# Optimization experiments

Measured on AMD Instinct MI355X. Metric: run time of the kernel, lower is better.

Reference implementation:

```python
import jax, jax.numpy as jnp
import numpy as np

MAX_LR = 0.01  # max_learning_rate
NS_A, NS_B, NS_C = 3.4445, -4.7750, 2.0315  # muon Newton-Schulz quintic coefficients


def newtonschulz5(G, steps=5, eps=1e-7):
    # Orthogonalize the last two dims of G (batched over leading dims).
    transpose = G.shape[-2] > G.shape[-1]
    X = jnp.swapaxes(G, -2, -1) if transpose else G
    X = X / (jnp.linalg.norm(X, axis=(-2, -1), keepdims=True) + eps)
    for _ in range(steps):
        A = X @ jnp.swapaxes(X, -2, -1)
        Bm = NS_B * A + NS_C * (A @ A)
        X = NS_A * X + Bm @ X
    return jnp.swapaxes(X, -2, -1) if transpose else X


def setup_inputs() -> dict:
    key = jax.random.key(0)
    ks = jax.random.split(key, 9)
    B, N, D, H, DH = 4, 1024, 1024, 8, 64
    s = D ** -0.5  # scale fast-weight init for numerical sanity (math unchanged)
    return {
        'tokens': jax.random.normal(ks[0], (B, N, D), jnp.float32),
        'wq': jax.random.normal(ks[1], (H, D, DH), jnp.float32) * s,
        'wk': jax.random.normal(ks[2], (H, D, DH), jnp.float32) * s,
        'wv': jax.random.normal(ks[3], (H, D, DH), jnp.float32) * s,
        'wo': jax.random.normal(ks[4], (H, DH, D), jnp.float32) * s,
        'w_lr': jax.random.normal(ks[5], (D, 2), jnp.float32) * 0.02,      # to_learning_rate (no bias)
        'w_target': jax.random.normal(ks[6], (D, D), jnp.float32) * 0.02,  # to_target_values linear (no bias)
        'w_gates': jax.random.normal(ks[7], (D, H), jnp.float32) * 0.02,   # to_gates linear (no bias)
        'rms_w': jnp.ones((D,), jnp.float32),                              # RMSNorm weight
    }


def reference(tokens, wq, wk, wv, wo, w_lr, w_target, w_gates, rms_w):
    N = tokens.shape[1]
    scale = wq.shape[-1] ** -0.5
    eps = jnp.finfo(tokens.dtype).eps

    # RMSNorm
    t = tokens * jax.lax.rsqrt(jnp.mean(tokens * tokens, -1, keepdims=True) + eps) * rms_w

    # gates: b n h -> b h n 1
    gates = jnp.swapaxes(jax.nn.sigmoid(t @ w_gates), -2, -1)[..., None]

    # per-batch fast weights == shared params (past_mem=None), broadcast over b via einsum
    q = jnp.einsum('bnd,hde->bhne', t, wq)
    k = jnp.einsum('bnd,hde->bhne', t, wk)
    v = jnp.einsum('bnd,hde->bhne', t, wv)

    score = jnp.einsum('bhie,bhje->bhij', q, k) * scale
    causal_mask = jnp.triu(jnp.ones((N, N), bool), 1)
    score = jnp.where(causal_mask, -jnp.finfo(score.dtype).max, score)
    attn = jax.nn.softmax(score, axis=-1)
    out = jnp.einsum('bhij,bhje->bhie', attn, v) * gates
    pred_values = jnp.einsum('bhne,hed->bnd', out, wo)

    # target values: linear + LayerNorm (no affine) on shifted tokens
    tv = t[:, 1:] @ w_target
    tv = (tv - tv.mean(-1, keepdims=True)) * jax.lax.rsqrt(tv.var(-1, keepdims=True) + 1e-5)

    # drop last position everywhere
    ts = t[:, :-1]
    pv = pred_values[:, :-1]
    o = out[:, :, :-1]
    g = gates[:, :, :-1]
    a = attn[:, :, :-1, :-1]
    qs, ks_, vs = q[:, :, :-1], k[:, :, :-1], v[:, :, :-1]

    lrs = jax.nn.sigmoid(ts @ w_lr) * MAX_LR  # b (n-1) 2
    lr, mlr = lrs[..., 0], lrs[..., 1]

    # hand-derived backward through the attention fast-weight readout
    error = tv - pv
    dout = jnp.einsum('bnd,hed->bhne', error, wo)
    du = dout * g
    delta = jnp.sum(dout * o, -1, keepdims=True)
    dv = jnp.einsum('bhij,bhie->bhje', a, du)
    dattn = jnp.einsum('bhje,bhie->bhij', vs, du)
    dscore = scale * a * (dattn - delta)
    dq = jnp.einsum('bhje,bhij->bhie', ks_, dscore)
    dk = jnp.einsum('bhie,bhij->bhje', qs, dscore)

    t_qk = ts * lr[..., None]
    t_v = ts * mlr[..., None]
    o_wo = o * mlr[:, None, :, None]

    dwq = jnp.einsum('bhie,bid->bhde', dq, t_qk)
    dwk = jnp.einsum('bhje,bjd->bhde', dk, t_qk)
    dwv = jnp.einsum('bhje,bjd->bhde', dv, t_v)
    dwo = jnp.einsum('bnd,bhne->bhed', error, o_wo)

    dwv = newtonschulz5(dwv)  # muon orthogonalization
    dwo = newtonschulz5(dwo)

    return pred_values, dwq, dwk, dwv, dwo
```

## Files before the change

### kernel.cpp

```cpp
#include <hip/hip_runtime.h>
#include <hip/hip_bf16.h>
#include <math.h>

#define BB 4
#define NN 1024
#define DD 1024
#define HH 8
#define DH 64
#define NSR 1023

#define NS_Ac 3.4445f
#define NS_Bc (-4.775f)
#define NS_Cc 2.0315f

typedef short bf16x8 __attribute__((ext_vector_type(8)));
typedef float f32x4 __attribute__((ext_vector_type(4)));
#define MFMA16(a,b,c) __builtin_amdgcn_mfma_f32_16x16x32_bf16(a,b,c,0,0,0)

#define QS 72
#define TS 40
#define GS 40

static __device__ __forceinline__ float ldin(const void* p, size_t i, int f) {
  return f ? ((const float*)p)[i] : __bfloat162float(((const __hip_bfloat16*)p)[i]);
}
static __device__ __forceinline__ void stout(void* p, size_t i, float v, int f) {
  if (f) ((float*)p)[i] = v;
  else   ((__hip_bfloat16*)p)[i] = __float2bfloat16(v);
}
static __device__ __forceinline__ short f2bs(float x) {
  union { float f; unsigned u; } a; a.f = x;
  unsigned r = a.u + 0x7fffu + ((a.u >> 16) & 1u);
  return (short)(r >> 16);
}
static __device__ __forceinline__ float bs2f(short s) {
  union { unsigned u; float f; } a; a.u = ((unsigned)(unsigned short)s) << 16;
  return a.f;
}
static __device__ __forceinline__ f32x4 fz4() { f32x4 z = {0.f,0.f,0.f,0.f}; return z; }
static __device__ __forceinline__ bf16x8 bz8() { bf16x8 z = {0,0,0,0,0,0,0,0}; return z; }

static __device__ __forceinline__ void mm64(const short* __restrict__ Ah, const short* __restrict__ Al,
                                            const short* __restrict__ Bh, const short* __restrict__ Bl,
                                            f32x4* acc, int w, int l15, int quad) {
#pragma unroll
  for (int kc = 0; kc < 64; kc += 32) {
    bf16x8 ah = *(const bf16x8*)&Ah[(w*16 + l15)*QS + kc + quad*8];
    bf16x8 al = *(const bf16x8*)&Al[(w*16 + l15)*QS + kc + quad*8];
#pragma unroll
    for (int es = 0; es < 4; es++) {
      bf16x8 bh = *(const bf16x8*)&Bh[(es*16 + l15)*QS + kc + quad*8];
      bf16x8 bl = *(const bf16x8*)&Bl[(es*16 + l15)*QS + kc + quad*8];
      acc[es] = MFMA16(ah, bh, acc[es]);
      acc[es] = MFMA16(ah, bl, acc[es]);
      acc[es] = MFMA16(al, bh, acc[es]);
    }
  }
}
static __device__ __forceinline__ void st_hl(short* __restrict__ Dh, short* __restrict__ Dl,
                                             const f32x4* v, int w, int l15, int quad) {
#pragma unroll
  for (int es = 0; es < 4; es++)
#pragma unroll
    for (int rr = 0; rr < 4; rr++) {
      int row = w*16 + quad*4 + rr, col = es*16 + l15;
      float x = v[es][rr];
      short h = f2bs(x);
      Dh[row*QS + col] = h;
      Dl[row*QS + col] = f2bs(x - bs2f(h));
    }
}

__global__ __launch_bounds__(256) void k_prep(
    const void* wq, const void* wk, const void* wv,
    const void* w_target, const void* wo, const void* w_lr, const void* w_gates, const void* rms_w,
    short* __restrict__ BqkvT, short* __restrict__ wtT, short* __restrict__ woT2,
    short* __restrict__ wo_bf, float* __restrict__ lrw, float* __restrict__ gw,
    float* __restrict__ rms_f, int* __restrict__ flag)
{
  const int f = (((const unsigned short*)rms_w)[0] == 0x3F80) ? 0 : 1;
  int bx = blockIdx.x; int tid = threadIdx.x;
  if (bx >= 768) {
    if (bx < 812) {
      if (bx == 768 && tid == 0) *flag = f;
      int idx = (bx - 768)*256 + tid;
      if (idx < 2048) lrw[idx] = ldin(w_lr, idx, f);
      else if (idx < 10240) gw[idx-2048] = ldin(w_gates, idx-2048, f);
      else if (idx < 11264) rms_f[idx-10240] = ldin(rms_w, idx-10240, f);
    } else {
      size_t base = (size_t)(bx - 812)*1024;
#pragma unroll
      for (int j = 0; j < 4; j++) {
        size_t i2 = base + tid + 256*j;
        wo_bf[i2] = f2bs(ldin(wo, i2, f));
      }
    }
    return;
  }
  const void* src; short* dst; int sld, dld, srow0, scol0, drow0; size_t soff = 0;
  if (bx < 384) {
    int x = bx & 15, y = bx >> 4;
    int n0 = y*64; int which = n0 >> 9, h = (n0 >> 6) & 7;
    src = (which==0) ? wq : (which==1) ? wk : wv;
    soff = (size_t)h*65536;
    sld = 64; dld = 1024; srow0 = x*64; scol0 = 0; drow0 = n0; dst = BqkvT;
  } else if (bx < 640) {
    int r = bx - 384; int x = r & 15, y = r >> 4;
    src = w_target; dst = wtT; sld = 1024; dld = 1024;
    srow0 = x*64; scol0 = y*64; drow0 = scol0;
  } else {
    int r = bx - 640; int x = r & 7, y = r >> 3;
    src = wo; dst = woT2; sld = 1024; dld = 512;
    srow0 = x*64; scol0 = y*64; drow0 = scol0;
  }
  __shared__ float T[64][65];
  int r4 = tid >> 4, c4 = (tid & 15)*4;
  for (int rr = r4; rr < 64; rr += 16)
#pragma unroll
    for (int j = 0; j < 4; j++)
      T[rr][c4+j] = ldin(src, soff + (size_t)(srow0+rr)*sld + scol0 + c4 + j, f);
  __syncthreads();
  int dc = tid >> 2, seg = tid & 3;
  bf16x8 o1, o2;
#pragma unroll
  for (int j = 0; j < 8; j++) { o1[j] = f2bs(T[seg*16+j][dc]); o2[j] = f2bs(T[seg*16+8+j][dc]); }
  *(bf16x8*)&dst[(size_t)(drow0+dc)*dld + srow0 + seg*16]     = o1;
  *(bf16x8*)&dst[(size_t)(drow0+dc)*dld + srow0 + seg*16 + 8] = o2;
}

__global__ __launch_bounds__(256) void k_transp(
    const float* __restrict__ src, size_t sStepZ, int sld,
    short* __restrict__ dst, size_t dStepZ, int dld,
    const float* __restrict__ coef, int zIsBh, int nz)
{
  int z = blockIdx.z;
  const float* sb = src + (size_t)z*sStepZ;
  short* db = dst + (size_t)z*dStepZ;
  const float* cb = coef ? coef + (size_t)(zIsBh ? (z>>3) : z)*1024 : (const float*)0;
  int x0 = blockIdx.x*64, y0 = blockIdx.y*64;
  __shared__ float T[64][65];
  int tid = threadIdx.x;
  int r4 = tid >> 4, c4 = (tid & 15)*4;
  for (int rr = r4; rr < 64; rr += 16) {
    int rg = x0 + rr;
    bool val = rg < nz;
    float cf = val ? (cb ? cb[rg] : 1.f) : 0.f;
    float4 v = val ? *(const float4*)&sb[(size_t)rg*sld + y0 + c4] : make_float4(0,0,0,0);
    T[rr][c4+0] = v.x*cf; T[rr][c4+1] = v.y*cf; T[rr][c4+2] = v.z*cf; T[rr][c4+3] = v.w*cf;
  }
  __syncthreads();
  int dc = tid >> 2, seg = tid & 3;
  bf16x8 o1, o2;
#pragma unroll
  for (int j = 0; j < 8; j++) { o1[j] = f2bs(T[seg*16+j][dc]); o2[j] = f2bs(T[seg*16+8+j][dc]); }
  *(bf16x8*)&db[(size_t)(y0+dc)*dld + x0 + seg*16]     = o1;
  *(bf16x8*)&db[(size_t)(y0+dc)*dld + x0 + seg*16 + 8] = o2;
}

__global__ __launch_bounds__(256) void k_transp5(
    const float* __restrict__ dq, const float* __restrict__ dk, const float* __restrict__ dv,
    const float* __restrict__ predf, const float* __restrict__ o,
    short* __restrict__ dqT, short* __restrict__ dkT, short* __restrict__ dvT,
    short* __restrict__ errT, short* __restrict__ oT,
    const float* __restrict__ lr, const float* __restrict__ mlr)
{
  int bx = blockIdx.x;
  const float* src; short* dst; const float* cb; int sld, dld, x0, y0;
  size_t sStep, dStep; int z;
  if (bx < 1536) {
    int which = bx >> 9; int r = bx & 511;
    z = r >> 4; x0 = (r & 15)*64; y0 = 0;
    sld = 64; dld = 1024; sStep = 65536; dStep = 65536;
    if (which == 0)      { src = dq; dst = dqT; cb = lr; }
    else if (which == 1) { src = dk; dst = dkT; cb = lr; }
    else                 { src = dv; dst = dvT; cb = mlr; }
    cb += (size_t)(z >> 3)*1024;
  } else if (bx < 2560) {
    int r = bx - 1536; z = r >> 8; x0 = (r & 15)*64; y0 = ((r >> 4) & 15)*64;
    src = predf; dst = errT; cb = (const float*)0;
    sld = 1024; dld = 1024; sStep = 1048576; dStep = 1048576;
  } else {
    int r = bx - 2560; z = r >> 7; x0 = (r & 15)*64; y0 = ((r >> 4) & 7)*64;
    src = o; dst = oT; cb = mlr + (size_t)z*1024;
    sld = 512; dld = 1024; sStep = 524288; dStep = 524288;
  }
  src += (size_t)z*sStep; dst += (size_t)z*dStep;
  __shared__ float T[64][65];
  int tid = threadIdx.x;
  int r4 = tid >> 4, c4 = (tid & 15)*4;
  for (int rr = r4; rr < 64; rr += 16) {
    int rg = x0 + rr;
    bool val = rg < 1023;
    float cf = val ? (cb ? cb[rg] : 1.f) : 0.f;
    float4 v = val ? *(const float4*)&src[(size_t)rg*sld + y0 + c4] : make_float4(0,0,0,0);
    T[rr][c4+0] = v.x*cf; T[rr][c4+1] = v.y*cf; T[rr][c4+2] = v.z*cf; T[rr][c4+3] = v.w*cf;
  }
  __syncthreads();
  int dc = tid >> 2, seg = tid & 3;
  bf16x8 o1, o2;
#pragma unroll
  for (int j = 0; j < 8; j++) { o1[j] = f2bs(T[seg*16+j][dc]); o2[j] = f2bs(T[seg*16+8+j][dc]); }
  *(bf16x8*)&dst[(size_t)(y0+dc)*dld + x0 + seg*16]     = o1;
  *(bf16x8*)&dst[(size_t)(y0+dc)*dld + x0 + seg*16 + 8] = o2;
}

__global__ void k_rmsnorm(const void* __restrict__ tokens, const float* __restrict__ rms_f,
                          const float* __restrict__ gw, const float* __restrict__ lrw,
                          float* __restrict__ t, short* __restrict__ t_bf,
                          float* __restrict__ gates, float* __restrict__ lr, float* __restrict__ mlr,
                          const int* __restrict__ flag) {
  const int f = *flag;
  int row = blockIdx.x;
  int b = row >> 10, n = row & 1023;
  __shared__ float red[256];
  __shared__ float red2[4][10];
  float xv[4]; float acc = 0.f;
#pragma unroll
  for (int i = 0; i < 4; i++) {
    xv[i] = ldin(tokens, (size_t)row*DD + threadIdx.x + 256*i, f);
    acc += xv[i]*xv[i];
  }
  red[threadIdx.x] = acc; __syncthreads();
  for (int s = 128; s > 0; s >>= 1) { if (threadIdx.x < s) red[threadIdx.x] += red[threadIdx.x+s]; __syncthreads(); }
  float r = rsqrtf(red[0] / DD + 1.1920929e-07f);
  float a10[10] = {0,0,0,0,0,0,0,0,0,0};
#pragma unroll
  for (int i = 0; i < 4; i++) {
    int d = threadIdx.x + 256*i;
    float v = xv[i] * r * rms_f[d];
    t[(size_t)row*DD + d] = v;
    t_bf[(size_t)row*DD + d] = f2bs(v);
#pragma unroll
    for (int h = 0; h < HH; h++) a10[h] += v * gw[d*HH + h];
    a10[8] += v * lrw[d*2];
    a10[9] += v * lrw[d*2+1];
  }
  int lane = threadIdx.x & 63, w = threadIdx.x >> 6;
#pragma unroll
  for (int c = 0; c < 10; c++) {
    float a = a10[c];
    for (int s = 32; s > 0; s >>= 1) a += __shfl_xor(a, s, 64);
    if (lane == 0) red2[w][c] = a;
  }
  __syncthreads();
  if (threadIdx.x < 10) {
    int c = threadIdx.x;
    float sum = red2[0][c]+red2[1][c]+red2[2][c]+red2[3][c];
    float sg = 1.f / (1.f + __expf(-sum));
    if (c < 8)      gates[((size_t)b*HH + c)*NN + n] = sg;
    else if (c == 8) lr[row]  = sg * 0.01f;
    else             mlr[row] = sg * 0.01f;
  }
}

__global__ __launch_bounds__(256) void k_gemm2(
    const short* __restrict__ A, const short* __restrict__ B,
    int lda, int ldb, int K, int M, int rowmode, int ep,
    float* __restrict__ O0, short* __restrict__ OS, void* __restrict__ OD,
    short* __restrict__ VT, const float* __restrict__ gates, const int* __restrict__ flag)
{
  int m0 = blockIdx.x*128, n0 = blockIdx.y*128;
  __shared__ __align__(16) short sm2[17408];
  short* As = sm2;
  short* Bs = sm2 + 5120;
  int tid = threadIdx.x;
  int lane = tid & 63, w = tid >> 6;
  int wr = w >> 1, wc = w & 1;
  int l15 = lane & 15, quad = lane >> 4;
  int row = tid >> 1, col16 = (tid & 1)*16;
  int r = m0 + row;
  int arow;
  if (rowmode == 1)      { int b = r / 1023; arow = r + b + 1; }
  else if (rowmode == 2) { int b = r / 1023; arow = r + b; }
  else arow = r;
  bool aval = (r < M);
  const short* Ap = A + (size_t)arow*lda + col16;
  const short* Bp = B + (size_t)(n0+row)*ldb + col16;
  f32x4 acc[4][4];
#pragma unroll
  for (int mi = 0; mi < 4; mi++)
#pragma unroll
    for (int ni = 0; ni < 4; ni++) acc[mi][ni] = fz4();
  bf16x8 av0 = aval ? *(const bf16x8*)(Ap) : bz8();
  bf16x8 av1 = aval ? *(const bf16x8*)(Ap + 8) : bz8();
  bf16x8 bv0 = *(const bf16x8*)(Bp);
  bf16x8 bv1 = *(const bf16x8*)(Bp + 8);
  for (int kb = 0; kb < K; kb += 32) {
    __syncthreads();
    *(bf16x8*)&As[row*GS + col16]     = av0;
    *(bf16x8*)&As[row*GS + col16 + 8] = av1;
    *(bf16x8*)&Bs[row*GS + col16]     = bv0;
    *(bf16x8*)&Bs[row*GS + col16 + 8] = bv1;
    __syncthreads();
    if (kb + 32 < K) {
      av0 = aval ? *(const bf16x8*)(Ap + kb + 32) : bz8();
      av1 = aval ? *(const bf16x8*)(Ap + kb + 40) : bz8();
      bv0 = *(const bf16x8*)(Bp + kb + 32);
      bv1 = *(const bf16x8*)(Bp + kb + 40);
    }
    bf16x8 afr[4], bfr[4];
#pragma unroll
    for (int mi = 0; mi < 4; mi++)
      afr[mi] = *(const bf16x8*)&As[(wr*64 + mi*16 + l15)*GS + quad*8];
#pragma unroll
    for (int ni = 0; ni < 4; ni++)
      bfr[ni] = *(const bf16x8*)&Bs[(wc*64 + ni*16 + l15)*GS + quad*8];
#pragma unroll
    for (int mi = 0; mi < 4; mi++)
#pragma unroll
      for (int ni = 0; ni < 4; ni++)
        acc[mi][ni] = MFMA16(afr[mi], bfr[ni], acc[mi][ni]);
  }
  const int f = flag ? *flag : 1;
#pragma unroll
  for (int mi = 0; mi < 4; mi++)
#pragma unroll
    for (int ni = 0; ni < 4; ni++)
#pragma unroll
      for (int rix = 0; rix < 4; rix++) {
        int rr = m0 + wr*64 + mi*16 + quad*4 + rix;
        if (rr >= M) continue;
        int c = n0 + wc*64 + ni*16 + l15;
        float val = acc[mi][ni][rix];
        if (ep == 0) {
          int which = c >> 9; int h = (c >> 6) & 7; int e = c & 63;
          int b = rr >> 10; int n = rr & 1023;
          OS[(size_t)which*2097152 + (((size_t)b*8 + h)*1024 + n)*64 + e] = f2bs(val);
        } else if (ep == 1) {
          O0[(size_t)rr*1024 + c] = val;
          stout(OD, (size_t)rr*1024 + c, val, f);
        } else if (ep == 2) {
          O0[(size_t)rr*1024 + c] = val;
        } else {
          int b = rr / 1023; int n = rr % 1023;
          int h = c >> 6;
          float g = gates[((size_t)b*8 + h)*1024 + n];
          OS[((size_t)b*1024 + n)*512 + c] = f2bs(val * g);
        }
      }
  if (ep == 0 && n0 >= 1024) {
    short* ST = sm2;
    __syncthreads();
#pragma unroll
    for (int mi = 0; mi < 4; mi++)
#pragma unroll
      for (int ni = 0; ni < 4; ni++)
#pragma unroll
        for (int rix = 0; rix < 4; rix++) {
          int ml = wr*64 + mi*16 + quad*4 + rix;
          int cl = wc*64 + ni*16 + l15;
          int mo = ml + ((ml >> 6) << 3);
          ST[cl*136 + mo] = f2bs(acc[mi][ni][rix]);
        }
    __syncthreads();
    int r2 = tid >> 1;
    int sg = tid & 1;
    int cg = n0 + r2;
    int h = (cg >> 6) & 7;
    int e = cg & 63;
    int b = m0 >> 10;
    int bh = b*8 + h;
    size_t dst = ((size_t)bh*64 + e)*1024 + (m0 & 1023) + sg*64;
    int so = r2*136 + sg*72;
#pragma unroll
    for (int j = 0; j < 64; j += 8)
      *(bf16x8*)&VT[dst + j] = *(const bf16x8*)&ST[so + j];
  }
}

__global__ __launch_bounds__(256) void k_gemm_bf(
    const short* __restrict__ A, const short* __restrict__ B,
    int lda, int ldb, int K, int M, int rowmode, int ep,
    size_t aStepBh, size_t aStepB, size_t bStepBh, size_t bStepB,
    float* __restrict__ O0, short* __restrict__ OS, void* __restrict__ OD,
    size_t out_off, const float* __restrict__ gates, const int* __restrict__ flag,
    const short* __restrict__ A2, const short* __restrict__ B2,
    size_t bStepB2, size_t out_off2, int ldb2)
{
  int z = blockIdx.z;
  const short* Au = A; const short* Bu = B;
  size_t bStepBv = bStepB; size_t out_offv = out_off;
  int epv = ep; int ldbv = ldb;
  if (ep == 4 && z >= 32) { Bu = B2; out_offv = out_off2; z -= 32; }
  if (ep == 5 && z >= 32) { Au = A2; Bu = B2; bStepBv = bStepB2; ldbv = ldb2; epv = 6; z -= 32; }
  int zb = z >> 3;
  const short* Ab = Au + (size_t)z*aStepBh + (size_t)zb*aStepB;
  const short* Bb = Bu + (size_t)z*bStepBh + (size_t)zb*bStepBv;
  int m0 = blockIdx.x*64, n0 = blockIdx.y*64;
  __shared__ __align__(16) short AsBs[5120];
  short* As = AsBs;
  short* Bs = AsBs + 2560;
  int tid = threadIdx.x;
  int lane = tid & 63, w = tid >> 6;
  int l15 = lane & 15, quad = lane >> 4;
  int row = tid >> 2, col8 = (tid & 3)*8;
  int r = m0 + row;
  int arow;
  if (rowmode == 1)      { int b = r / 1023; arow = r + b + 1; }
  else if (rowmode == 2) { int b = r / 1023; arow = r + b; }
  else arow = r;
  bool aval = (r < M);
  const short* Ap = Ab + (size_t)arow*lda + col8;
  const short* Bp = Bb + (size_t)(n0+row)*ldbv + col8;
  f32x4 acc[4] = {fz4(),fz4(),fz4(),fz4()};
  bf16x8 av = aval ? *(const bf16x8*)(Ap) : bz8();
  bf16x8 bv = *(const bf16x8*)(Bp);
  for (int kb = 0; kb < K; kb += 32) {
    __syncthreads();
    *(bf16x8*)&As[row*GS + col8] = av;
    *(bf16x8*)&Bs[row*GS + col8] = bv;
    __syncthreads();
    if (kb + 32 < K) {
      av = aval ? *(const bf16x8*)(Ap + kb + 32) : bz8();
      bv = *(const bf16x8*)(Bp + kb + 32);
    }
    bf16x8 afr = *(const bf16x8*)&As[(w*16 + l15)*GS + quad*8];
#pragma unroll
    for (int es = 0; es < 4; es++) {
      bf16x8 bfr = *(const bf16x8*)&Bs[(es*16 + l15)*GS + quad*8];
      acc[es] = MFMA16(afr, bfr, acc[es]);
    }
  }
  const int f = flag ? *flag : 1;
#pragma unroll
  for (int es = 0; es < 4; es++) {
#pragma unroll
    for (int rix = 0; rix < 4; rix++) {
      int rr = m0 + w*16 + quad*4 + rix;
      if (rr >= M) continue;
      int c = n0 + es*16 + l15;
      float val = acc[es][rix];
      if (epv == 4) {
        stout(OD, out_offv + ((size_t)z*1024 + rr)*64 + c, val, f);
      } else if (epv == 5) {
        O0[((size_t)z*64 + rr)*1024 + c] = val;
      } else if (epv == 6) {
        O0[((size_t)(32 + z)*64 + rr)*1024 + c] = val;
      }
    }
  }
}

__global__ __launch_bounds__(256) void k_attn_fwd(
    const short* __restrict__ qb, const short* __restrict__ kb, const short* __restrict__ vbT,
    const float* __restrict__ gates,
    float* __restrict__ o, short* __restrict__ o_bf,
    float* __restrict__ mrow, float* __restrict__ lrow)
{
  int pp = blockIdx.x >> 8;
  int xx = (blockIdx.x >> 5) & 7;
  int bh = blockIdx.x & 31;
  int it = pp ? xx : (15 - xx);
  int i0 = it*64;
  int b = bh >> 3, h = bh & 7;
  __shared__ __align__(16) short Qs[64*QS];
  __shared__ __align__(16) short Ks[32*QS];
  __shared__ __align__(16) short VsT[64*TS];
  __shared__ __align__(16) short Ps[64*TS];
  int tid = threadIdx.x;
  int lane = tid & 63, w = tid >> 6;
  int l15 = lane & 15, quad = lane >> 4;
  int sr = tid >> 3, sc = (tid & 7) * 8;
  int sr2 = tid >> 2, sc2 = (tid & 3) * 8;
  int rsw = (l15 >> 2) & 3;
  for (int rr = sr; rr < 64; rr += 32)
    *(bf16x8*)&Qs[rr*QS + sc] = *(const bf16x8*)&qb[((size_t)bh*1024 + i0 + rr)*64 + sc];
  f32x4 oa[4] = {fz4(),fz4(),fz4(),fz4()};
  float m_st[4] = {-1e30f,-1e30f,-1e30f,-1e30f};
  float l_st[4] = {0.f,0.f,0.f,0.f};
  int jiters = 2*it + 2;
  bf16x8 rk = *(const bf16x8*)&kb[((size_t)bh*1024 + sr)*64 + sc];
  bf16x8 rv = *(const bf16x8*)&vbT[((size_t)bh*64 + sr2)*1024 + sc2];
  for (int jc = 0; jc < jiters; jc++) {
    int j0 = jc*32;
    __syncthreads();
    *(bf16x8*)&Ks[sr*QS + sc]    = rk;
    *(bf16x8*)&VsT[sr2*TS + sc2] = rv;
    __syncthreads();
    if (jc + 1 < jiters) {
      int j1 = j0 + 32;
      rk = *(const bf16x8*)&kb[((size_t)bh*1024 + j1 + sr)*64 + sc];
      rv = *(const bf16x8*)&vbT[((size_t)bh*64 + sr2)*1024 + j1 + sc2];
    }
    f32x4 sa[2] = {fz4(),fz4()};
#pragma unroll
    for (int kc = 0; kc < 64; kc += 32) {
      bf16x8 afr = *(const bf16x8*)&Qs[(w*16 + l15)*QS + kc + quad*8];
#pragma unroll
      for (int ni = 0; ni < 2; ni++) {
        bf16x8 bfr = *(const bf16x8*)&Ks[(ni*16 + l15)*QS + kc + quad*8];
        sa[ni] = MFMA16(afr, bfr, sa[ni]);
      }
    }
#pragma unroll
    for (int r = 0; r < 4; r++) {
      int gi = i0 + w*16 + quad*4 + r;
      float s0 = sa[0][r]*0.125f, s1 = sa[1][r]*0.125f;
      if (j0 + l15 > gi)      s0 = -1e30f;
      if (j0 + 16 + l15 > gi) s1 = -1e30f;
      float rm = fmaxf(s0, s1);
      rm = fmaxf(rm, __shfl_xor(rm, 1, 64));
      rm = fmaxf(rm, __shfl_xor(rm, 2, 64));
      rm = fmaxf(rm, __shfl_xor(rm, 4, 64));
      rm = fmaxf(rm, __shfl_xor(rm, 8, 64));
      float m_new = fmaxf(m_st[r], rm);
      float alpha = __expf(m_st[r] - m_new);
      float p0 = __expf(s0 - m_new), p1 = __expf(s1 - m_new);
      float rs = p0 + p1;
      rs += __shfl_xor(rs, 1, 64);
      rs += __shfl_xor(rs, 2, 64);
      rs += __shfl_xor(rs, 4, 64);
      rs += __shfl_xor(rs, 8, 64);
      l_st[r] = l_st[r]*alpha + rs;
      m_st[r] = m_new;
#pragma unroll
      for (int es = 0; es < 4; es++) oa[es][r] *= alpha;
      int rowp = w*16 + quad*4 + r;
      int lo3 = l15 & 7, g0 = l15 >> 3;
      Ps[rowp*TS + ((( g0      ^ quad) << 3) | lo3)] = f2bs(p0);
      Ps[rowp*TS + ((((g0 | 2) ^ quad) << 3) | lo3)] = f2bs(p1);
    }
    bf16x8 pa = *(const bf16x8*)&Ps[(w*16 + l15)*TS + ((quad ^ rsw) << 3)];
#pragma unroll
    for (int es = 0; es < 4; es++) {
      bf16x8 bv = *(const bf16x8*)&VsT[(es*16 + l15)*TS + quad*8];
      oa[es] = MFMA16(pa, bv, oa[es]);
    }
  }
#pragma unroll
  for (int r = 0; r < 4; r++) {
    int gi = i0 + w*16 + quad*4 + r;
    float g = gates[(size_t)bh*1024 + gi] / l_st[r];
#pragma unroll
    for (int es = 0; es < 4; es++) {
      float val = oa[es][r] * g;
      size_t oi = ((size_t)b*1024 + gi)*512 + h*64 + es*16 + l15;
      o[oi] = val;
      o_bf[oi] = f2bs(val);
    }
    if (l15 == 0) {
      mrow[(size_t)bh*1024 + gi] = m_st[r];
      lrow[(size_t)bh*1024 + gi] = l_st[r];
    }
  }
}

__global__ void k_lnsub(const float* __restrict__ tvbuf, float* __restrict__ predf,
                        short* __restrict__ err_bf) {
  int r = blockIdx.x; int b = r / 1023; int prow = r + b;
  const float* tvr = tvbuf + (size_t)r*1024;
  __shared__ float red[256];
  float s1 = 0.f, s2 = 0.f;
  float xv[4];
#pragma unroll
  for (int i = 0; i < 4; i++) {
    xv[i] = tvr[threadIdx.x + 256*i];
    s1 += xv[i]; s2 += xv[i]*xv[i];
  }
  red[threadIdx.x] = s1; __syncthreads();
  for (int s = 128; s > 0; s >>= 1){ if (threadIdx.x < s) red[threadIdx.x] += red[threadIdx.x+s]; __syncthreads(); }
  float mean = red[0] / 1024.f; __syncthreads();
  red[threadIdx.x] = s2; __syncthreads();
  for (int s = 128; s > 0; s >>= 1){ if (threadIdx.x < s) red[threadIdx.x] += red[threadIdx.x+s]; __syncthreads(); }
  float var = red[0]/1024.f - mean*mean;
  float rstd = rsqrtf(var + 1e-5f);
  float* er = predf + (size_t)prow*1024;
#pragma unroll
  for (int i = 0; i < 4; i++) {
    int d = threadIdx.x + 256*i;
    float e = (xv[i]-mean)*rstd - er[d];
    er[d] = e;
    err_bf[(size_t)prow*1024 + d] = f2bs(e);
  }
// ... 405 lines not shown
    __syncthreads();
  }
#pragma unroll
  for (int es = 0; es < 4; es++)
#pragma unroll
    for (int rr = 0; rr < 4; rr++) {
      int row = w*16 + quad*4 + rr, col = es*16 + l15;
      M5[(size_t)m*4096 + row*64 + col] = bs2f(Mhi[row*QS + col]) + bs2f(Mlo[row*QS + col]);
    }
  if (tid == 0) rbuf[m] = r_;
}

__global__ __launch_bounds__(256) void k_ns_apply(const float* __restrict__ Xsrc, const float* __restrict__ M5,
                                                  const float* __restrict__ rbuf, void* __restrict__ d_outv,
                                                  size_t off_dwv, size_t off_dwo, const int* __restrict__ flag) {
  int m = blockIdx.x, cs = blockIdx.y;
  const float* Xm = Xsrc + (size_t)m*DH*DD;
  const int f = *flag;
  float r_ = rbuf[m];
  __shared__ __align__(16) short Mhi[4608], Mlo[4608], XThi[4608], XTlo[4608];
  __shared__ float Sf[64*65];
  int tid = threadIdx.x;
  int lane = tid & 63, w = tid >> 6;
  int l15 = lane & 15, quad = lane >> 4;
  int srow = tid >> 2, scol = (tid & 3)*8;
  for (int i = tid; i < 4096; i += 256) {
    float v = M5[(size_t)m*4096 + i];
    int rowi = i >> 6, coli = i & 63;
    short h = f2bs(v);
    Mhi[rowi*QS + coli] = h;
    Mlo[rowi*QS + coli] = f2bs(v - bs2f(h));
  }
  int cbase = cs*256;
  float4 d1 = *(const float4*)&Xm[(size_t)srow*1024 + cbase + scol];
  float4 d2 = *(const float4*)&Xm[(size_t)srow*1024 + cbase + scol + 4];
  float4 d3 = *(const float4*)&Xm[(size_t)srow*1024 + cbase + scol + 32];
  float4 d4 = *(const float4*)&Xm[(size_t)srow*1024 + cbase + scol + 36];
  for (int cc = 0; cc < 256; cc += 64) {
    int c0 = cbase + cc;
    __syncthreads();
    {
      float xv0[8] = {d1.x,d1.y,d1.z,d1.w,d2.x,d2.y,d2.z,d2.w};
      float xv1[8] = {d3.x,d3.y,d3.z,d3.w,d4.x,d4.y,d4.z,d4.w};
#pragma unroll
      for (int j = 0; j < 8; j++) {
        int n0 = scol + j;
        short h0 = f2bs(xv0[j]);
        XThi[n0*QS + srow] = h0;
        XTlo[n0*QS + srow] = f2bs(xv0[j] - bs2f(h0));
        int n1 = scol + 32 + j;
        short h1 = f2bs(xv1[j]);
        XThi[n1*QS + srow] = h1;
        XTlo[n1*QS + srow] = f2bs(xv1[j] - bs2f(h1));
      }
    }
    __syncthreads();
    if (cc + 64 < 256) {
      d1 = *(const float4*)&Xm[(size_t)srow*1024 + c0 + 64 + scol];
      d2 = *(const float4*)&Xm[(size_t)srow*1024 + c0 + 64 + scol + 4];
      d3 = *(const float4*)&Xm[(size_t)srow*1024 + c0 + 64 + scol + 32];
      d4 = *(const float4*)&Xm[(size_t)srow*1024 + c0 + 64 + scol + 36];
    }
    f32x4 u4[4] = {fz4(),fz4(),fz4(),fz4()};
    mm64(Mhi, Mlo, XThi, XTlo, u4, w, l15, quad);
    if (m >= 32) {
#pragma unroll
      for (int es = 0; es < 4; es++)
#pragma unroll
        for (int rr = 0; rr < 4; rr++) {
          int row = w*16 + quad*4 + rr, col = c0 + es*16 + l15;
          stout(d_outv, off_dwo + (size_t)(m-32)*65536 + (size_t)row*1024 + col, r_*u4[es][rr], f);
        }
    } else {
#pragma unroll
      for (int es = 0; es < 4; es++)
#pragma unroll
        for (int rr = 0; rr < 4; rr++) {
          int row = w*16 + quad*4 + rr, col = es*16 + l15;
          Sf[col*65 + row] = r_*u4[es][rr];
        }
      __syncthreads();
      int dl = tid >> 2, e0 = (tid & 3)*16;
      size_t ob = off_dwv + (size_t)m*65536 + (size_t)(c0 + dl)*64 + e0;
#pragma unroll
      for (int j = 0; j < 16; j++)
        stout(d_outv, ob + j, Sf[dl*65 + e0 + j], f);
    }
  }
}

extern "C" void kernel_launch(void* const* d_in, const int* in_sizes, int n_in,
                              void* d_out, int out_size, void* d_ws, size_t ws_size,
                              hipStream_t stream) {
  const void* tokens   = d_in[0];
  const void* wq       = d_in[1];
  const void* wk       = d_in[2];
  const void* wv       = d_in[3];
  const void* wo       = d_in[4];
  const void* w_lr     = d_in[5];
  const void* w_target = d_in[6];
  const void* w_gates  = d_in[7];
  const void* rms_w    = d_in[8];

  const size_t off_dwq  = 4194304;
  const size_t off_dwk  = 6291456;
  const size_t off_dwv  = 8388608;
  const size_t off_dwo  = 10485760;

  float* ws = (float*)d_ws;
  float* t_    = ws;
  float* tvbuf = ws;
  short* errT  = (short*)ws;
  short* oT    = (short*)(ws + 2097152);
  short* t_bf  = (short*)(ws + 4194304);
  short* err_bf= (short*)(ws + 4194304);
  short* tT    = (short*)(ws + 6291456);
  short* qb    = (short*)(ws + 8388608);
  short* kbuf  = qb + 2097152;
  short* vbuf  = qb + 4194304;
  short* dqT   = (short*)(ws + 8388608);
  short* dkT   = dqT + 2097152;
  short* dvT   = dqT + 4194304;
  float* o_    = ws + 11534336;
  short* o_bf  = (short*)(ws + 13631488);
  short* du_bf = (short*)(ws + 13631488);
  float* predf = ws + 14680064;
  float* Xns   = ws + 14680064;
  short* BqkvT = (short*)(ws + 18874368);
  short* wtT   = (short*)(ws + 19660800);
  short* woT2  = (short*)(ws + 20185088);
  short* wo_bf = (short*)(ws + 20447232);
  float* gw    = ws + 20709376;
  float* lrw   = ws + 20717568;
  float* rms_f = ws + 20719616;
  float* dv_   = ws + 18874368;
  float* dk_   = ws + 20971520;
  float* dq_   = ws + 23068672;
  float* gates_= ws + 25165824;
  float* mrow_ = ws + 25198592;
  float* lrow_ = ws + 25231360;
  float* delta_= ws + 25264128;
  float* lr_   = ws + 25296896;
  float* mlr_  = ws + 25300992;
  int*   flag_ = (int*)(ws + 25305088);
  short* vbT = (short*)(ws + 3145728);
  short* duT = (short*)(ws + 3145728);
  short* kbT = (short*)(ws + 4194304);
  short* qbT = (short*)ws;
  float* Gpart  = ws + 18874368;
  float* M5b    = ws + 19922944;
  float* rbuf   = ws + 20185088;
  float* sspart = ws + 20185152;

  hipLaunchKernelGGL(k_prep, dim3(1324), dim3(256), 0, stream, wq, wk, wv, w_target, wo, w_lr, w_gates, rms_w,
                     BqkvT, wtT, woT2, wo_bf, lrw, gw, rms_f, flag_);
  hipLaunchKernelGGL(k_rmsnorm, dim3(BB*NN), dim3(256), 0, stream, tokens, rms_f, gw, lrw,
                     t_, t_bf, gates_, lr_, mlr_, flag_);
  hipLaunchKernelGGL(k_transp, dim3(64,16,1), dim3(256), 0, stream, t_, (size_t)0, 1024, tT, (size_t)0, 4096, (const float*)nullptr, 0, 4096);

  hipLaunchKernelGGL(k_gemm2, dim3(32,12), dim3(256), 0, stream, t_bf, BqkvT, 1024, 1024, 1024, 4096, 0, 0,
                     (float*)nullptr, qb, (void*)nullptr, vbT, (const float*)nullptr, flag_);
  hipLaunchKernelGGL(k_attn_fwd, dim3(512), dim3(256), 0, stream, qb, kbuf, vbT, gates_, o_, o_bf, mrow_, lrow_);
  hipLaunchKernelGGL(k_gemm2, dim3(32,8), dim3(256), 0, stream, o_bf, woT2, 512, 512, 512, 4096, 0, 1,
                     predf, (short*)nullptr, d_out, (short*)nullptr, (const float*)nullptr, flag_);
  hipLaunchKernelGGL(k_gemm2, dim3(32,8), dim3(256), 0, stream, t_bf, wtT, 1024, 1024, 1024, 4092, 1, 2,
                     tvbuf, (short*)nullptr, (void*)nullptr, (short*)nullptr, (const float*)nullptr, flag_);
  hipLaunchKernelGGL(k_lnsub, dim3(BB*NSR), dim3(256), 0, stream, tvbuf, predf, err_bf);
  hipLaunchKernelGGL(k_gemm2, dim3(32,4), dim3(256), 0, stream, err_bf, wo_bf, 1024, 1024, 1024, 4092, 2, 3,
                     (float*)nullptr, du_bf, (void*)nullptr, (short*)nullptr, gates_, flag_);
  hipLaunchKernelGGL(k_t16, dim3(1536 + BB*NSR), dim3(256), 0, stream, (const short*)qb, (const short*)du_bf,
                     kbT, duT, qbT, o_, gates_, delta_);
  hipLaunchKernelGGL(k_bwd, dim3(1024), dim3(256), 0, stream, qb, kbuf, vbuf, du_bf, qbT, duT, kbT,
                     mrow_, lrow_, delta_, dv_, dk_, dq_);
  hipLaunchKernelGGL(k_transp5, dim3(3072), dim3(256), 0, stream, dq_, dk_, dv_, predf, o_,
                     dqT, dkT, dvT, errT, oT, lr_, mlr_);
  hipLaunchKernelGGL(k_gemm_bf, dim3(16,1,64), dim3(256), 0, stream, tT, dqT, 4096, 1024, 1024, 1024, 0, 4,
                     (size_t)0,(size_t)1024,(size_t)65536,(size_t)0, (float*)nullptr, (short*)nullptr, d_out, off_dwq,
                     (const float*)nullptr, flag_, (const short*)nullptr, (const short*)dkT, (size_t)0, off_dwk, 1024);
  hipLaunchKernelGGL(k_gemm_bf, dim3(1,16,64), dim3(256), 0, stream, dvT, tT, 1024, 4096, 1024, 64, 0, 5,
                     (size_t)65536,(size_t)0,(size_t)0,(size_t)1024, Xns, (short*)nullptr, (void*)nullptr, (size_t)0,
                     (const float*)nullptr, flag_, (const short*)oT, (const short*)errT, (size_t)1048576, (size_t)0, 1024);
  hipLaunchKernelGGL(k_ns_g,     dim3(64,4), dim3(256), 0, stream, Xns, Gpart, sspart);
  hipLaunchKernelGGL(k_ns_iter,  dim3(64),   dim3(256), 0, stream, Gpart, sspart, M5b, rbuf);
  hipLaunchKernelGGL(k_ns_apply, dim3(64,4), dim3(256), 0, stream, Xns, M5b, rbuf, d_out, off_dwv, off_dwo, flag_);
  (void)in_sizes; (void)n_in; (void)out_size; (void)ws_size;
}
```

Baseline: 471.3 us.

## Merge rmsnorm into prep, batch two GEMMs in one launch, deepen k-tile

The RMSNorm/gates/lr work becomes extra blocks of the prep kernel and reads raw weights through ldin, so it no longer waits on the converted copies. The pred-values GEMM and the target-values GEMM now run in one launch, split on blockIdx.y. The batched bf16 GEMM moves from a 32-wide to a 64-wide k-step with larger shared tiles. Together these cut launch count and sync overhead and raise work per barrier, at the cost of more shared memory and possible occupancy loss in the bf16 GEMM.

```diff
diff --git a/kernel.cpp b/kernel.cpp
--- a/kernel.cpp
+++ b/kernel.cpp
@@ -76,10 +76,56 @@
     const void* w_target, const void* wo, const void* w_lr, const void* w_gates, const void* rms_w,
     short* __restrict__ BqkvT, short* __restrict__ wtT, short* __restrict__ woT2,
     short* __restrict__ wo_bf, float* __restrict__ lrw, float* __restrict__ gw,
-    float* __restrict__ rms_f, int* __restrict__ flag)
+    float* __restrict__ rms_f, int* __restrict__ flag,
+    const void* tokens, float* __restrict__ t, short* __restrict__ t_bf,
+    float* __restrict__ gates, float* __restrict__ lr, float* __restrict__ mlr)
 {
   const int f = (((const unsigned short*)rms_w)[0] == 0x3F80) ? 0 : 1;
   int bx = blockIdx.x; int tid = threadIdx.x;
+  if (bx >= 1324) {
+    int row = bx - 1324;
+    int b = row >> 10, n = row & 1023;
+    __shared__ float red[256];
+    __shared__ float red2[4][10];
+    float xv[4]; float acc = 0.f;
+#pragma unroll
+    for (int i = 0; i < 4; i++) {
+      xv[i] = ldin(tokens, (size_t)row*DD + tid + 256*i, f);
+      acc += xv[i]*xv[i];
+    }
+    red[tid] = acc; __syncthreads();
+    for (int s = 128; s > 0; s >>= 1) { if (tid < s) red[tid] += red[tid+s]; __syncthreads(); }
+    float r = rsqrtf(red[0] / DD + 1.1920929e-07f);
+    float a10[10] = {0,0,0,0,0,0,0,0,0,0};
+#pragma unroll
+    for (int i = 0; i < 4; i++) {
+      int d = tid + 256*i;
+      float v = xv[i] * r * ldin(rms_w, d, f);
+      t[(size_t)row*DD + d] = v;
+      t_bf[(size_t)row*DD + d] = f2bs(v);
+#pragma unroll
+      for (int h = 0; h < HH; h++) a10[h] += v * ldin(w_gates, (size_t)d*HH + h, f);
+      a10[8] += v * ldin(w_lr, (size_t)d*2, f);
+      a10[9] += v * ldin(w_lr, (size_t)d*2 + 1, f);
+    }
+    int lane = tid & 63, w = tid >> 6;
+#pragma unroll
+    for (int c = 0; c < 10; c++) {
+      float a = a10[c];
+      for (int s = 32; s > 0; s >>= 1) a += __shfl_xor(a, s, 64);
+      if (lane == 0) red2[w][c] = a;
+    }
+    __syncthreads();
+    if (tid < 10) {
+      int c = tid;
+      float sum = red2[0][c]+red2[1][c]+red2[2][c]+red2[3][c];
+      float sg = 1.f / (1.f + __expf(-sum));
+      if (c < 8)      gates[((size_t)b*HH + c)*NN + n] = sg;
+      else if (c == 8) lr[row]  = sg * 0.01f;
+      else             mlr[row] = sg * 0.01f;
+    }
+    return;
+  }
   if (bx >= 768) {
     if (bx < 812) {
       if (bx == 768 && tid == 0) *flag = f;
@@ -204,62 +250,24 @@
   *(bf16x8*)&dst[(size_t)(y0+dc)*dld + x0 + seg*16 + 8] = o2;
 }
 
-__global__ void k_rmsnorm(const void* __restrict__ tokens, const float* __restrict__ rms_f,
-                          const float* __restrict__ gw, const float* __restrict__ lrw,
-                          float* __restrict__ t, short* __restrict__ t_bf,
-                          float* __restrict__ gates, float* __restrict__ lr, float* __restrict__ mlr,
-                          const int* __restrict__ flag) {
-  const int f = *flag;
-  int row = blockIdx.x;
-  int b = row >> 10, n = row & 1023;
-  __shared__ float red[256];
-  __shared__ float red2[4][10];
-  float xv[4]; float acc = 0.f;
-#pragma unroll
-  for (int i = 0; i < 4; i++) {
-    xv[i] = ldin(tokens, (size_t)row*DD + threadIdx.x + 256*i, f);
-    acc += xv[i]*xv[i];
-  }
-  red[threadIdx.x] = acc; __syncthreads();
-  for (int s = 128; s > 0; s >>= 1) { if (threadIdx.x < s) red[threadIdx.x] += red[threadIdx.x+s]; __syncthreads(); }
-  float r = rsqrtf(red[0] / DD + 1.1920929e-07f);
-  float a10[10] = {0,0,0,0,0,0,0,0,0,0};
-#pragma unroll
-  for (int i = 0; i < 4; i++) {
-    int d = threadIdx.x + 256*i;
-    float v = xv[i] * r * rms_f[d];
-    t[(size_t)row*DD + d] = v;
-    t_bf[(size_t)row*DD + d] = f2bs(v);
-#pragma unroll
-    for (int h = 0; h < HH; h++) a10[h] += v * gw[d*HH + h];
-    a10[8] += v * lrw[d*2];
-    a10[9] += v * lrw[d*2+1];
-  }
-  int lane = threadIdx.x & 63, w = threadIdx.x >> 6;
-#pragma unroll
-  for (int c = 0; c < 10; c++) {
-    float a = a10[c];
-    for (int s = 32; s > 0; s >>= 1) a += __shfl_xor(a, s, 64);
-    if (lane == 0) red2[w][c] = a;
-  }
-  __syncthreads();
-  if (threadIdx.x < 10) {
-    int c = threadIdx.x;
-    float sum = red2[0][c]+red2[1][c]+red2[2][c]+red2[3][c];
-    float sg = 1.f / (1.f + __expf(-sum));
-    if (c < 8)      gates[((size_t)b*HH + c)*NN + n] = sg;
-    else if (c == 8) lr[row]  = sg * 0.01f;
-    else             mlr[row] = sg * 0.01f;
-  }
-}
-
 __global__ __launch_bounds__(256) void k_gemm2(
     const short* __restrict__ A, const short* __restrict__ B,
     int lda, int ldb, int K, int M, int rowmode, int ep,
     float* __restrict__ O0, short* __restrict__ OS, void* __restrict__ OD,
-    short* __restrict__ VT, const float* __restrict__ gates, const int* __restrict__ flag)
+    short* __restrict__ VT, const float* __restrict__ gates, const int* __restrict__ flag,
+    int ysplit, const short* __restrict__ A2, const short* __restrict__ B2,
+    int lda2, int ldb2, int K2, int M2, int rowmode2, int ep2p,
+    float* __restrict__ O02, void* __restrict__ OD2)
 {
-  int m0 = blockIdx.x*128, n0 = blockIdx.y*128;
+  int yb = blockIdx.y;
+  const short* Au = A; const short* Bu = B;
+  int ldav = lda, ldbv = ldb, Kv = K, Mv = M, rmv = rowmode, epv = ep;
+  float* O0v = O0; void* ODv = OD;
+  if (ysplit && yb >= ysplit) {
+    yb -= ysplit; Au = A2; Bu = B2; ldav = lda2; ldbv = ldb2; Kv = K2; Mv = M2;
+    rmv = rowmode2; epv = ep2p; O0v = O02; ODv = OD2;
+  }
+  int m0 = blockIdx.x*128, n0 = yb*128;
   __shared__ __align__(16) short sm2[17408];
   short* As = sm2;
   short* Bs = sm2 + 5120;
@@ -270,12 +278,12 @@
   int row = tid >> 1, col16 = (tid & 1)*16;
   int r = m0 + row;
   int arow;
-  if (rowmode == 1)      { int b = r / 1023; arow = r + b + 1; }
-  else if (rowmode == 2) { int b = r / 1023; arow = r + b; }
+  if (rmv == 1)      { int b = r / 1023; arow = r + b + 1; }
+  else if (rmv == 2) { int b = r / 1023; arow = r + b; }
   else arow = r;
-  bool aval = (r < M);
-  const short* Ap = A + (size_t)arow*lda + col16;
-  const short* Bp = B + (size_t)(n0+row)*ldb + col16;
+  bool aval = (r < Mv);
+  const short* Ap = Au + (size_t)arow*ldav + col16;
+  const short* Bp = Bu + (size_t)(n0+row)*ldbv + col16;
   f32x4 acc[4][4];
 #pragma unroll
   for (int mi = 0; mi < 4; mi++)
@@ -285,14 +293,14 @@
   bf16x8 av1 = aval ? *(const bf16x8*)(Ap + 8) : bz8();
   bf16x8 bv0 = *(const bf16x8*)(Bp);
   bf16x8 bv1 = *(const bf16x8*)(Bp + 8);
-  for (int kb = 0; kb < K; kb += 32) {
+  for (int kb = 0; kb < Kv; kb += 32) {
     __syncthreads();
     *(bf16x8*)&As[row*GS + col16]     = av0;
     *(bf16x8*)&As[row*GS + col16 + 8] = av1;
     *(bf16x8*)&Bs[row*GS + col16]     = bv0;
     *(bf16x8*)&Bs[row*GS + col16 + 8] = bv1;
     __syncthreads();
-    if (kb + 32 < K) {
+    if (kb + 32 < Kv) {
       av0 = aval ? *(const bf16x8*)(Ap + kb + 32) : bz8();
       av1 = aval ? *(const bf16x8*)(Ap + kb + 40) : bz8();
       bv0 = *(const bf16x8*)(Bp + kb + 32);
@@ -319,18 +327,18 @@
 #pragma unroll
       for (int rix = 0; rix < 4; rix++) {
         int rr = m0 + wr*64 + mi*16 + quad*4 + rix;
-        if (rr >= M) continue;
+        if (rr >= Mv) continue;
         int c = n0 + wc*64 + ni*16 + l15;
         float val = acc[mi][ni][rix];
-        if (ep == 0) {
+        if (epv == 0) {
           int which = c >> 9; int h = (c >> 6) & 7; int e = c & 63;
           int b = rr >> 10; int n = rr & 1023;
           OS[(size_t)which*2097152 + (((size_t)b*8 + h)*1024 + n)*64 + e] = f2bs(val);
-        } else if (ep == 1) {
-          O0[(size_t)rr*1024 + c] = val;
-          stout(OD, (size_t)rr*1024 + c, val, f);
-        } else if (ep == 2) {
-          O0[(size_t)rr*1024 + c] = val;
+        } else if (epv == 1) {
+          O0v[(size_t)rr*1024 + c] = val;
+          stout(ODv, (size_t)rr*1024 + c, val, f);
+        } else if (epv == 2) {
+          O0v[(size_t)rr*1024 + c] = val;
         } else {
           int b = rr / 1023; int n = rr % 1023;
           int h = c >> 6;
@@ -338,7 +346,7 @@
           OS[((size_t)b*1024 + n)*512 + c] = f2bs(val * g);
         }
       }
-  if (ep == 0 && n0 >= 1024) {
+  if (epv == 0 && n0 >= 1024) {
     short* ST = sm2;
     __syncthreads();
 #pragma unroll
@@ -387,38 +395,47 @@
   const short* Ab = Au + (size_t)z*aStepBh + (size_t)zb*aStepB;
   const short* Bb = Bu + (size_t)z*bStepBh + (size_t)zb*bStepBv;
   int m0 = blockIdx.x*64, n0 = blockIdx.y*64;
-  __shared__ __align__(16) short AsBs[5120];
+  __shared__ __align__(16) short AsBs[9216];
   short* As = AsBs;
-  short* Bs = AsBs + 2560;
+  short* Bs = AsBs + 4608;
   int tid = threadIdx.x;
   int lane = tid & 63, w = tid >> 6;
   int l15 = lane & 15, quad = lane >> 4;
-  int row = tid >> 2, col8 = (tid & 3)*8;
+  int row = tid >> 2, col16 = (tid & 3)*16;
   int r = m0 + row;
   int arow;
   if (rowmode == 1)      { int b = r / 1023; arow = r + b + 1; }
   else if (rowmode == 2) { int b = r / 1023; arow = r + b; }
   else arow = r;
   bool aval = (r < M);
-  const short* Ap = Ab + (size_t)arow*lda + col8;
-  const short* Bp = Bb + (size_t)(n0+row)*ldbv + col8;
+  const short* Ap = Ab + (size_t)arow*lda + col16;
+  const short* Bp = Bb + (size_t)(n0+row)*ldbv + col16;
   f32x4 acc[4] = {fz4(),fz4(),fz4(),fz4()};
-  bf16x8 av = aval ? *(const bf16x8*)(Ap) : bz8();
-  bf16x8 bv = *(const bf16x8*)(Bp);
-  for (int kb = 0; kb < K; kb += 32) {
-    __syncthreads();
-    *(bf16x8*)&As[row*GS + col8] = av;
-    *(bf16x8*)&Bs[row*GS + col8] = bv;
-    __syncthreads();
-    if (kb + 32 < K) {
-      av = aval ? *(const bf16x8*)(Ap + kb + 32) : bz8();
-      bv = *(const bf16x8*)(Bp + kb + 32);
-    }
-    bf16x8 afr = *(const bf16x8*)&As[(w*16 + l15)*GS + quad*8];
-#pragma unroll
-    for (int es = 0; es < 4; es++) {
-      bf16x8 bfr = *(const bf16x8*)&Bs[(es*16 + l15)*GS + quad*8];
-      acc[es] = MFMA16(afr, bfr, acc[es]);
+  bf16x8 av0 = aval ? *(const bf16x8*)(Ap) : bz8();
+  bf16x8 av1 = aval ? *(const bf16x8*)(Ap + 8) : bz8();
+  bf16x8 bv0 = *(const bf16x8*)(Bp);
+  bf16x8 bv1 = *(const bf16x8*)(Bp + 8);
+  for (int kb = 0; kb < K; kb += 64) {
+    __syncthreads();
+    *(bf16x8*)&As[row*QS + col16]     = av0;
+    *(bf16x8*)&As[row*QS + col16 + 8] = av1;
+    *(bf16x8*)&Bs[row*QS + col16]     = bv0;
+    *(bf16x8*)&Bs[row*QS + col16 + 8] = bv1;
+    __syncthreads();
+    if (kb + 64 < K) {
+      av0 = aval ? *(const bf16x8*)(Ap + kb + 64) : bz8();
+      av1 = aval ? *(const bf16x8*)(Ap + kb + 72) : bz8();
+      bv0 = *(const bf16x8*)(Bp + kb + 64);
+      bv1 = *(const bf16x8*)(Bp + kb + 72);
+    }
+#pragma unroll
+    for (int kc = 0; kc < 64; kc += 32) {
+      bf16x8 afr = *(const bf16x8*)&As[(w*16 + l15)*QS + kc + quad*8];
+#pragma unroll
+      for (int es = 0; es < 4; es++) {
+        bf16x8 bfr = *(const bf16x8*)&Bs[(es*16 + l15)*QS + kc + quad*8];
+        acc[es] = MFMA16(afr, bfr, acc[es]);
+      }
     }
   }
   const int f = flag ? *flag : 1;
@@ -1130,22 +1147,22 @@
   float* rbuf   = ws + 20185088;
   float* sspart = ws + 20185152;
 
-  hipLaunchKernelGGL(k_prep, dim3(1324), dim3(256), 0, stream, wq, wk, wv, w_target, wo, w_lr, w_gates, rms_w,
-                     BqkvT, wtT, woT2, wo_bf, lrw, gw, rms_f, flag_);
-  hipLaunchKernelGGL(k_rmsnorm, dim3(BB*NN), dim3(256), 0, stream, tokens, rms_f, gw, lrw,
-                     t_, t_bf, gates_, lr_, mlr_, flag_);
+  hipLaunchKernelGGL(k_prep, dim3(1324 + BB*NN), dim3(256), 0, stream, wq, wk, wv, w_target, wo, w_lr, w_gates, rms_w,
+                     BqkvT, wtT, woT2, wo_bf, lrw, gw, rms_f, flag_,
+                     tokens, t_, t_bf, gates_, lr_, mlr_);
   hipLaunchKernelGGL(k_transp, dim3(64,16,1), dim3(256), 0, stream, t_, (size_t)0, 1024, tT, (size_t)0, 4096, (const float*)nullptr, 0, 4096);
 
   hipLaunchKernelGGL(k_gemm2, dim3(32,12), dim3(256), 0, stream, t_bf, BqkvT, 1024, 1024, 1024, 4096, 0, 0,
-                     (float*)nullptr, qb, (void*)nullptr, vbT, (const float*)nullptr, flag_);
+                     (float*)nullptr, qb, (void*)nullptr, vbT, (const float*)nullptr, flag_,
+                     0, (const short*)nullptr, (const short*)nullptr, 0, 0, 0, 0, 0, 0, (float*)nullptr, (void*)nullptr);
   hipLaunchKernelGGL(k_attn_fwd, dim3(512), dim3(256), 0, stream, qb, kbuf, vbT, gates_, o_, o_bf, mrow_, lrow_);
-  hipLaunchKernelGGL(k_gemm2, dim3(32,8), dim3(256), 0, stream, o_bf, woT2, 512, 512, 512, 4096, 0, 1,
-                     predf, (short*)nullptr, d_out, (short*)nullptr, (const float*)nullptr, flag_);
-  hipLaunchKernelGGL(k_gemm2, dim3(32,8), dim3(256), 0, stream, t_bf, wtT, 1024, 1024, 1024, 4092, 1, 2,
-                     tvbuf, (short*)nullptr, (void*)nullptr, (short*)nullptr, (const float*)nullptr, flag_);
+  hipLaunchKernelGGL(k_gemm2, dim3(32,16), dim3(256), 0, stream, o_bf, woT2, 512, 512, 512, 4096, 0, 1,
+                     predf, (short*)nullptr, d_out, (short*)nullptr, (const float*)nullptr, flag_,
+                     8, t_bf, wtT, 1024, 1024, 1024, 4092, 1, 2, tvbuf, (void*)nullptr);
   hipLaunchKernelGGL(k_lnsub, dim3(BB*NSR), dim3(256), 0, stream, tvbuf, predf, err_bf);
   hipLaunchKernelGGL(k_gemm2, dim3(32,4), dim3(256), 0, stream, err_bf, wo_bf, 1024, 1024, 1024, 4092, 2, 3,
-                     (float*)nullptr, du_bf, (void*)nullptr, (short*)nullptr, gates_, flag_);
+                     (float*)nullptr, du_bf, (void*)nullptr, (short*)nullptr, gates_, flag_,
+                     0, (const short*)nullptr, (const short*)nullptr, 0, 0, 0, 0, 0, 0, (float*)nullptr, (void*)nullptr);
   hipLaunchKernelGGL(k_t16, dim3(1536 + BB*NSR), dim3(256), 0, stream, (const short*)qb, (const short*)du_bf,
                      kbT, duT, qbT, o_, gates_, delta_);
   hipLaunchKernelGGL(k_bwd, dim3(1024), dim3(256), 0, stream, qb, kbuf, vbuf, du_bf, qbT, duT, kbT,
```

Result: slower. 550.3 us (+16.8%).
